# Optimization experiments

Hardware: AMD Instinct MI355X
Metric: run time of the kernel (lower is better)

The kernel has to match this reference:

```python
import jax, jax.numpy as jnp
import numpy as np

B, T, D, H = 2, 2048, 768, 12
HS = D // H


def setup_inputs() -> dict:
    key = jax.random.key(0)
    ks = jax.random.split(key, 11)
    s = 1.0 / np.sqrt(D)
    return {
        "query": jax.random.normal(ks[0], (B, T, D), jnp.float32),
        "key": jax.random.normal(ks[1], (B, T, D), jnp.float32),
        "value": jax.random.normal(ks[2], (B, T, D), jnp.float32),
        "Wq": jax.random.normal(ks[3], (D, D), jnp.float32) * s,
        "bq": jax.random.normal(ks[4], (D,), jnp.float32) * s,
        "Wk": jax.random.normal(ks[5], (D, D), jnp.float32) * s,
        "bk": jax.random.normal(ks[6], (D,), jnp.float32) * s,
        "Wv": jax.random.normal(ks[7], (D, D), jnp.float32) * s,
        "bv": jax.random.normal(ks[8], (D,), jnp.float32) * s,
        "Wo": jax.random.normal(ks[9], (D, D), jnp.float32) * s,
        "bo": jax.random.normal(ks[10], (D,), jnp.float32) * s,
    }


def reference(query, key, value, Wq, bq, Wk, bk, Wv, bv, Wo, bo):
    # Projections (torch nn.Linear: x @ W.T + b), then split heads -> [B,H,T,HS]
    def split_heads(x):
        return x.reshape(B, -1, H, HS).transpose(0, 2, 1, 3)

    q = split_heads(query @ Wq.T + bq)
    k = split_heads(key @ Wk.T + bk)
    v = split_heads(value @ Wv.T + bv)

    scale = 1.0 / jnp.sqrt(jnp.asarray(HS, q.dtype))
    scores = jnp.einsum("bhqd,bhkd->bhqk", q, k) * scale  # [B,H,Tq,Tk]
    attn = jax.nn.softmax(scores, axis=-1)
    out = jnp.einsum("bhqk,bhkd->bhqd", attn, v)  # [B,H,Tq,HS]
    out = out.transpose(0, 2, 1, 3).reshape(B, -1, D)
    output = out @ Wo.T + bo
    return output, attn.mean(axis=1)
```

## Files before the change

### kernel.cpp

```cpp
#include <hip/hip_runtime.h>
#include <hip/hip_fp16.h>
#include <stdint.h>

typedef _Float16 f16;
typedef _Float16 f16x8 __attribute__((ext_vector_type(8)));
typedef _Float16 f16x4v __attribute__((ext_vector_type(4)));
typedef __fp16 h16x2 __attribute__((ext_vector_type(2)));
typedef float f32x4 __attribute__((ext_vector_type(4)));
typedef float f32x16 __attribute__((ext_vector_type(16)));

#define MFMA16(a,b,c) __builtin_amdgcn_mfma_f32_16x16x32_f16(a,b,c,0,0,0)
#define MFMA32(a,b,c) __builtin_amdgcn_mfma_f32_32x32x16_f16(a,b,c,0,0,0)
#define CVTPK(a,b) __builtin_amdgcn_cvt_pkrtz(a,b)

#if __has_builtin(__builtin_amdgcn_exp2f)
#define EXP2(x) __builtin_amdgcn_exp2f(x)
#else
#define EXP2(x) exp2f(x)
#endif

static __device__ __forceinline__ float dot2acc(h16x2 a, float c) {
#if __has_builtin(__builtin_amdgcn_fdot2)
    const h16x2 one = { (__fp16)1.f, (__fp16)1.f };
    return __builtin_amdgcn_fdot2(a, one, c, false);
#else
    return c + (float)a[0] + (float)a[1];
#endif
}

typedef __attribute__((address_space(1))) void gvoid_t;
typedef __attribute__((address_space(3))) void svoid_t;
#define AS1(p) ((gvoid_t*)(uintptr_t)(p))
#define AS3(p) ((svoid_t*)(uint32_t)(uintptr_t)(p))

static constexpr int Bc = 2, Tc = 2048, Dc = 768, Hc = 12;
static constexpr int Mc = Bc * Tc;
static constexpr float SC2 = 0.18033688011112042f;

union PA { f16x8 v; h16x2 h[4]; };

#define FRAG32(BASE, ROWOFF, CHUNK) \
    (*(const f16x8*)((const char*)(BASE) + \
        ((ROWOFF) + q32) * 128 + (((CHUNK) ^ g7) * 16)))

__global__ __launch_bounds__(256) void conv_all(
    const float* __restrict__ q, const float* __restrict__ k, const float* __restrict__ v,
    const float* __restrict__ wq, const float* __restrict__ wk, const float* __restrict__ wv,
    const float* __restrict__ wo,
    f16* __restrict__ qh, f16* __restrict__ kh, f16* __restrict__ vh,
    f16* __restrict__ wqh, f16* __restrict__ wkh, f16* __restrict__ wvh, f16* __restrict__ woh)
{
    const int NI = (Mc * Dc) / 4;
    const int NW = (Dc * Dc) / 4;
    int i = blockIdx.x * 256 + threadIdx.x;
    if (i >= 3 * NI + 4 * NW) return;
    const float4* src; f16* dst; int j; float scl = 1.f;
    if (i < 3 * NI) {
        int a = i / NI; j = i - a * NI;
        src = (const float4*)(a == 0 ? q : (a == 1 ? k : v));
        dst = (a == 0 ? qh : (a == 1 ? kh : vh));
    } else {
        int t = i - 3 * NI;
        int a = t / NW; j = t - a * NW;
        src = (const float4*)(a == 0 ? wq : (a == 1 ? wk : (a == 2 ? wv : wo)));
        dst = (a == 0 ? wqh : (a == 1 ? wkh : (a == 2 ? wvh : woh)));
        if (a == 0) scl = SC2;
    }
    float4 f = src[j];
    f16x4v o = { (f16)(f.x * scl), (f16)(f.y * scl), (f16)(f.z * scl), (f16)(f.w * scl) };
    *(f16x4v*)(dst + 4 * j) = o;
}

__device__ __forceinline__ void gemm_tile_mainloop_db(
    const f16* __restrict__ A, const f16* __restrict__ W,
    int brow, int bcol, f16* As, f16* Bs, f32x4 acc[4][4])
{
    const int tid = threadIdx.x;
    const int w = tid >> 6, lane = tid & 63;
    const int lg = lane & 15, hg = lane >> 4;
    const int wr = w >> 1, wc = w & 1;

#define GS(KT_, BUF_) do { \
    const int k0_ = (KT_) * 32; \
    _Pragma("unroll") \
    for (int j_ = 0; j_ < 2; ++j_) { \
        int p_ = (w * 2 + j_) * 1024 + lane * 16; \
        int r_ = p_ >> 6; \
        int ke_ = (p_ & 63) >> 1; \
        __builtin_amdgcn_global_load_lds(AS1(A + (size_t)(brow + r_) * 768 + k0_ + ke_), \
            AS3((char*)As + (BUF_) * 8192 + (w * 2 + j_) * 1024), 16, 0, 0); \
        __builtin_amdgcn_global_load_lds(AS1(W + (size_t)(bcol + r_) * 768 + k0_ + ke_), \
            AS3((char*)Bs + (BUF_) * 8192 + (w * 2 + j_) * 1024), 16, 0, 0); \
    } } while (0)

    GS(0, 0);
    __syncthreads();
    for (int kt = 0; kt < 24; ++kt) {
        const int cur = kt & 1;
        if (kt < 23) GS(kt + 1, cur ^ 1);
        const f16* As_ = As + cur * 4096;
        const f16* Bs_ = Bs + cur * 4096;
        f16x8 af[4], bf[4];
#pragma unroll
        for (int m = 0; m < 4; ++m)
            af[m] = *(const f16x8*)(As_ + (wr * 64 + m * 16 + lg) * 32 + hg * 8);
#pragma unroll
        for (int n = 0; n < 4; ++n)
            bf[n] = *(const f16x8*)(Bs_ + (wc * 64 + n * 16 + lg) * 32 + hg * 8);
#pragma unroll
        for (int m = 0; m < 4; ++m)
#pragma unroll
            for (int n = 0; n < 4; ++n)
                acc[m][n] = MFMA16(af[m], bf[n], acc[m][n]);
        __syncthreads();
    }
#undef GS
}

__global__ __launch_bounds__(256) void qkv_proj(
    const f16* __restrict__ qh, const f16* __restrict__ kh, const f16* __restrict__ vh,
    const f16* __restrict__ wqh, const f16* __restrict__ wkh, const f16* __restrict__ wvh,
    const float* __restrict__ bq, const float* __restrict__ bk, const float* __restrict__ bv,
    f16* __restrict__ Qp, f16* __restrict__ Kp, f16* __restrict__ Vt)
{
    __shared__ f16 As[2][4096], Bs[2][4096];
    const int z = blockIdx.z;
    const f16* A = (z == 0) ? qh : (z == 1) ? kh : vh;
    const f16* W = (z == 0) ? wqh : (z == 1) ? wkh : wvh;
    const float* bias = (z == 0) ? bq : (z == 1) ? bk : bv;
    const int brow = blockIdx.y * 128, bcol = blockIdx.x * 128;

    f32x4 acc[4][4];
    const f32x4 z4 = { 0.f, 0.f, 0.f, 0.f };
#pragma unroll
    for (int m = 0; m < 4; ++m)
#pragma unroll
        for (int n = 0; n < 4; ++n) acc[m][n] = z4;

    gemm_tile_mainloop_db(A, W, brow, bcol, &As[0][0], &Bs[0][0], acc);

    const int tid = threadIdx.x, w = tid >> 6, lane = tid & 63;
    const int lg = lane & 15, hg = lane >> 4, wr = w >> 1, wc = w & 1;
#pragma unroll
    for (int n = 0; n < 4; ++n) {
        const int c = bcol + wc * 64 + n * 16 + lg;
        const float bval = (z == 0) ? bias[c] * SC2 : bias[c];
#pragma unroll
        for (int m = 0; m < 4; ++m) {
            const int r0 = brow + wr * 64 + m * 16 + hg * 4;
#pragma unroll
            for (int r = 0; r < 4; ++r) {
                const float val = acc[m][n][r] + bval;
                const int row = r0 + r;
                if (z == 0) {
                    Qp[(size_t)row * 768 + c] = (f16)val;
                } else if (z == 1) {
                    Kp[(size_t)row * 768 + c] = (f16)val;
                } else {
                    const int bb = row >> 11, t = row & 2047;
                    const int hh = c >> 6, d = c & 63;
                    const int tl = t & 31;
                    const int sw = ((tl >> 2) ^ (tl >> 3)) & 1;
                    const int tp = (t & ~31) | (tl ^ (sw * 12));
                    Vt[(((size_t)(bb * 12 + hh)) * 64 + d) * 2048 + tp] = (f16)val;
                }
            }
        }
    }
}

__global__ __launch_bounds__(256, 3) void attn_out(
    const f16* __restrict__ Qp, const f16* __restrict__ Kp, const f16* __restrict__ Vt,
    float* __restrict__ l_inv, f16* __restrict__ ctx)
{
    __shared__ f16 Kbuf[2][4096];
    __shared__ f16 Vbuf[2][4096];
    __shared__ float Ored[2][32][64];
    __shared__ float lred[2][2][32];

    const int qt = blockIdx.x, h = blockIdx.y, b = blockIdx.z;
    const int tid = threadIdx.x, w = tid >> 6, lane = tid & 63;
    const int q32 = lane & 31, hi = lane >> 5, g7 = lane & 7;
    const int qh = w & 1, kh = w >> 1;
    const int wbase16 = (tid & ~63) * 16;

    const size_t qrow0 = (size_t)b * 2048 + qt * 64 + qh * 32;
    const int hcol = h * 64;

    const f16* qb = Qp + (qrow0 + q32) * 768 + hcol + hi * 8;
    f16x8 bqf[4];
#pragma unroll
    for (int d = 0; d < 4; ++d) bqf[d] = *(const f16x8*)(qb + d * 16);

    const size_t kbase = (size_t)b * 2048;
    const f16* Vg = Vt + ((size_t)(b * 12 + h)) * 64 * 2048;

    f32x16 oacc[2];
#pragma unroll
    for (int dt = 0; dt < 2; ++dt)
#pragma unroll
        for (int r = 0; r < 16; ++r) oacc[dt][r] = 0.f;
    float lsum = 0.f;

#define STAGE_KV(KT_, BUF) do { \
    _Pragma("unroll") \
    for (int j_ = 0; j_ < 2; ++j_) { \
        const int p_ = j_ * 256 + tid; \
        const int row_ = p_ >> 3, c_ = (p_ & 7) ^ (row_ & 7); \
        __builtin_amdgcn_global_load_lds( \
            AS1(Kp + (kbase + (size_t)(KT_) * 64 + row_) * 768 + hcol + c_ * 8), \
            AS3((char*)&Kbuf[BUF][0] + j_ * 4096 + wbase16), 16, 0, 0); \
        __builtin_amdgcn_global_load_lds( \
            AS1(Vg + (size_t)row_ * 2048 + (KT_) * 64 + c_ * 8), \
            AS3((char*)&Vbuf[BUF][0] + j_ * 4096 + wbase16), 16, 0, 0); \
    } } while (0)

#define AOBODY(CUR) do { \
    const f16* Kb_ = &Kbuf[CUR][0]; const f16* Vb_ = &Vbuf[CUR][0]; \
    f32x16 sa; \
    _Pragma("unroll") \
    for (int r_ = 0; r_ < 16; ++r_) sa[r_] = 0.f; \
    sa = MFMA32(FRAG32(Kb_, kh * 32, 0 + hi), bqf[0], sa); \
    sa = MFMA32(FRAG32(Kb_, kh * 32, 2 + hi), bqf[1], sa); \
    sa = MFMA32(FRAG32(Kb_, kh * 32, 4 + hi), bqf[2], sa); \
    sa = MFMA32(FRAG32(Kb_, kh * 32, 6 + hi), bqf[3], sa); \
    float p[16]; \
    _Pragma("unroll") \
    for (int r_ = 0; r_ < 16; ++r_) p[r_] = EXP2(sa[r_]); \
    PA pa0, pa1; \
    pa0.h[0] = CVTPK(p[0], p[1]);   pa0.h[1] = CVTPK(p[2], p[3]); \
    pa0.h[2] = CVTPK(p[4], p[5]);   pa0.h[3] = CVTPK(p[6], p[7]); \
    pa1.h[0] = CVTPK(p[8], p[9]);   pa1.h[1] = CVTPK(p[10], p[11]); \
    pa1.h[2] = CVTPK(p[12], p[13]); pa1.h[3] = CVTPK(p[14], p[15]); \
    float t0_ = 0.f, t1_ = 0.f; \
    t0_ = dot2acc(pa0.h[0], t0_); t0_ = dot2acc(pa0.h[1], t0_); \
    t0_ = dot2acc(pa0.h[2], t0_); t0_ = dot2acc(pa0.h[3], t0_); \
    t1_ = dot2acc(pa1.h[0], t1_); t1_ = dot2acc(pa1.h[1], t1_); \
    t1_ = dot2acc(pa1.h[2], t1_); t1_ = dot2acc(pa1.h[3], t1_); \
    lsum += t0_ + t1_; \
    oacc[0] = MFMA32(FRAG32(Vb_, 0,  kh * 4 + 0 + hi), pa0.v, oacc[0]); \
    oacc[0] = MFMA32(FRAG32(Vb_, 0,  kh * 4 + 2 + hi), pa1.v, oacc[0]); \
    oacc[1] = MFMA32(FRAG32(Vb_, 32, kh * 4 + 0 + hi), pa0.v, oacc[1]); \
    oacc[1] = MFMA32(FRAG32(Vb_, 32, kh * 4 + 2 + hi), pa1.v, oacc[1]); \
} while (0)

    STAGE_KV(0, 0);
    __syncthreads();
    for (int kt = 0; kt < 32; ++kt) {
        const int cur = kt & 1;
        if (kt < 31) STAGE_KV(kt + 1, cur ^ 1);
        AOBODY(cur);
        __syncthreads();
    }
#undef STAGE_KV
#undef AOBODY

    lsum += __shfl_xor(lsum, 32);
    if (hi == 0) lred[kh][qh][q32] = lsum;
    if (kh == 1) {
#pragma unroll
        for (int dt = 0; dt < 2; ++dt)
#pragma unroll
            for (int g = 0; g < 4; ++g) {
                float4 v4 = { oacc[dt][g * 4 + 0], oacc[dt][g * 4 + 1],
                              oacc[dt][g * 4 + 2], oacc[dt][g * 4 + 3] };
                *(float4*)&Ored[qh][q32][dt * 32 + g * 8 + hi * 4] = v4;
            }
    }
    __syncthreads();
    if (kh == 0) {
        const float iv = 1.f / (lred[0][qh][q32] + lred[1][qh][q32]);
        if (hi == 0)
            l_inv[((size_t)(b * 12 + h)) * 2048 + qt * 64 + qh * 32 + q32] = iv;
        f16* cb = ctx + (qrow0 + q32) * 768 + hcol;
#pragma unroll
        for (int dt = 0; dt < 2; ++dt)
#pragma unroll
            for (int g = 0; g < 4; ++g) {
                const int d0 = dt * 32 + g * 8 + hi * 4;
                const float4 o4 = *(const float4*)&Ored[qh][q32][d0];
                f16x4v s;
#pragma unroll
                for (int e = 0; e < 4; ++e)
                    s[e] = (f16)((oacc[dt][g * 4 + e] + (&o4.x)[e]) * iv);
                *(f16x4v*)(cb + d0) = s;
            }
    }
}

__global__ __launch_bounds__(256) void tail_fused(
    const f16* __restrict__ ctx, const f16* __restrict__ woh,
    const float* __restrict__ bo, float* __restrict__ out,
    const f16* __restrict__ Qp, const f16* __restrict__ Kp,
    const float* __restrict__ l_inv, float* __restrict__ om)
{
    __shared__ f16 sh[4][4096];

    const int tid = threadIdx.x, w = tid >> 6, lane = tid & 63;

    if (blockIdx.x < 192) {
        const int brow = (blockIdx.x / 6) * 128, bcol = (blockIdx.x % 6) * 128;
        f32x4 acc[4][4];
        const f32x4 z4 = { 0.f, 0.f, 0.f, 0.f };
#pragma unroll
        for (int m = 0; m < 4; ++m)
#pragma unroll
            for (int n = 0; n < 4; ++n) acc[m][n] = z4;

        gemm_tile_mainloop_db(ctx, woh, brow, bcol, &sh[0][0], &sh[2][0], acc);

        const int lg = lane & 15, hg = lane >> 4, wr = w >> 1, wc = w & 1;
#pragma unroll
        for (int n = 0; n < 4; ++n) {
            const int c = bcol + wc * 64 + n * 16 + lg;
            const float bval = bo[c];
#pragma unroll
            for (int m = 0; m < 4; ++m) {
                const int r0 = brow + wr * 64 + m * 16 + hg * 4;
#pragma unroll
                for (int r = 0; r < 4; ++r)
                    out[(size_t)(r0 + r) * 768 + c] = acc[m][n][r] + bval;
            }
        }
    } else {
        const int mb = blockIdx.x - 192;
        const int kt = mb & 31, r2 = mb >> 5;
        const int qt = r2 & 31, b = r2 >> 5;
        const int q32 = lane & 31, hi = lane >> 5, g7 = lane & 7;
        const int qh = w & 1, kh = w >> 1;
        const int wbase16 = (tid & ~63) * 16;

        const size_t qtrow = (size_t)b * 2048 + qt * 64;
        const size_t ktrow = (size_t)b * 2048 + kt * 64;

        f32x16 macc;
#pragma unroll
        for (int r = 0; r < 16; ++r) macc[r] = 0.f;

#define MSTAGE(H_, BUF) do { \
    _Pragma("unroll") \
    for (int j_ = 0; j_ < 2; ++j_) { \
        const int p_ = j_ * 256 + tid; \
        const int row_ = p_ >> 3, c_ = (p_ & 7) ^ (row_ & 7); \
        __builtin_amdgcn_global_load_lds( \
            AS1(Qp + (qtrow + row_) * 768 + (H_) * 64 + c_ * 8), \
            AS3((char*)&sh[0][0] + (BUF) * 8192 + j_ * 4096 + wbase16), 16, 0, 0); \
        __builtin_amdgcn_global_load_lds( \
            AS1(Kp + (ktrow + row_) * 768 + (H_) * 64 + c_ * 8), \
            AS3((char*)&sh[2][0] + (BUF) * 8192 + j_ * 4096 + wbase16), 16, 0, 0); \
    } } while (0)

#define MBODY(H_, CUR) do { \
    const f16* Qb_ = (const f16*)((const char*)&sh[0][0] + (CUR) * 8192); \
    const f16* Kb_ = (const f16*)((const char*)&sh[2][0] + (CUR) * 8192); \
    f16x8 qf[4]; \
    _Pragma("unroll") \
    for (int d_ = 0; d_ < 4; ++d_) qf[d_] = FRAG32(Qb_, qh * 32, d_ * 2 + hi); \
    f32x16 sa; \
    _Pragma("unroll") \
    for (int r_ = 0; r_ < 16; ++r_) sa[r_] = 0.f; \
    sa = MFMA32(FRAG32(Kb_, kh * 32, 0 + hi), qf[0], sa); \
    sa = MFMA32(FRAG32(Kb_, kh * 32, 2 + hi), qf[1], sa); \
    sa = MFMA32(FRAG32(Kb_, kh * 32, 4 + hi), qf[2], sa); \
    sa = MFMA32(FRAG32(Kb_, kh * 32, 6 + hi), qf[3], sa); \
    const float ivv = l_inv[((size_t)(b * 12 + (H_))) * 2048 + qt * 64 + qh * 32 + q32]; \
    _Pragma("unroll") \
    for (int r_ = 0; r_ < 16; ++r_) macc[r_] += EXP2(sa[r_]) * ivv; \
} while (0)

        MSTAGE(0, 0);
        __syncthreads();
        for (int h = 0; h < 12; ++h) {
            const int cur = h & 1;
            if (h < 11) MSTAGE(h + 1, cur ^ 1);
            MBODY(h, cur);
            __syncthreads();
        }
#undef MSTAGE
#undef MBODY

        float* ob = om + ((size_t)(b * 2048 + qt * 64 + qh * 32 + q32)) * 2048
                  + kt * 64 + kh * 32;
#pragma unroll
        for (int g = 0; g < 4; ++g) {
            float4 v4 = { macc[g * 4 + 0] * (1.0f / 12.0f),
                          macc[g * 4 + 1] * (1.0f / 12.0f),
                          macc[g * 4 + 2] * (1.0f / 12.0f),
                          macc[g * 4 + 3] * (1.0f / 12.0f) };
            *(float4*)(ob + g * 8 + hi * 4) = v4;
        }
    }
}

extern "C" void kernel_launch(void* const* d_in, const int* in_sizes, int n_in,
                              void* d_out, int out_size, void* d_ws, size_t ws_size,
                              hipStream_t stream) {
    const float* q  = (const float*)d_in[0];
    const float* k  = (const float*)d_in[1];
    const float* v  = (const float*)d_in[2];
    const float* Wq = (const float*)d_in[3];
    const float* bq = (const float*)d_in[4];
    const float* Wk = (const float*)d_in[5];
    const float* bk = (const float*)d_in[6];
    const float* Wv = (const float*)d_in[7];
    const float* bv = (const float*)d_in[8];
    const float* Wo = (const float*)d_in[9];
    const float* bo = (const float*)d_in[10];
    float* out = (float*)d_out;

    char* ws = (char*)d_ws;
    const size_t SZ_IN = (size_t)Mc * Dc * 2;
    const size_t SZ_W  = (size_t)Dc * Dc * 2;
    f16* qh  = (f16*)(ws);
    f16* kh  = (f16*)(ws + SZ_IN);
    f16* vh  = (f16*)(ws + 2 * SZ_IN);
    f16* wqh = (f16*)(ws + 3 * SZ_IN);
    f16* wkh = (f16*)(ws + 3 * SZ_IN + SZ_W);
    f16* wvh = (f16*)(ws + 3 * SZ_IN + 2 * SZ_W);
    f16* woh = (f16*)(ws + 3 * SZ_IN + 3 * SZ_W);
    f16* Qp  = (f16*)(ws + 3 * SZ_IN + 4 * SZ_W);
    f16* Kp  = (f16*)(ws + 4 * SZ_IN + 4 * SZ_W);
    f16* Vt  = (f16*)(ws + 5 * SZ_IN + 4 * SZ_W);
    f16* ctx = qh;
    float* l_inv = (float*)kh;

    conv_all<<<dim3(11520), dim3(256), 0, stream>>>(q, k, v, Wq, Wk, Wv, Wo,
                                                    qh, kh, vh, wqh, wkh, wvh, woh);
    qkv_proj<<<dim3(6, 32, 3), dim3(256), 0, stream>>>(qh, kh, vh, wqh, wkh, wvh,
                                                       bq, bk, bv, Qp, Kp, Vt);
    attn_out<<<dim3(32, 12, 2), dim3(256), 0, stream>>>(Qp, Kp, Vt, l_inv, ctx);
    tail_fused<<<dim3(2240), dim3(256), 0, stream>>>(ctx, woh, bo, out,
                                                     Qp, Kp, l_inv,
                                                     out + (size_t)Mc * Dc);
}
```

Measured before the change: 131.2 us.

## Switch projection GEMMs to 32x32 MFMA with K=64 staging; widen head-mean tiles to 128 keys

The shared projection GEMM mainloop now stages 64-wide K slices with XOR-swizzled LDS layout and uses 32x32x16 MFMA fragments instead of 16x16x32, halving the number of K iterations and barriers. The attention-mean part of the tail kernel now processes 128 key columns per block, reusing each loaded Q head tile for two score tiles and roughly halving the block count. The changes aim to cut LDS traffic per FLOP, barrier count and redundant Q loads, at the cost of doubled LDS per block (which may reduce occupancy) and different epilogue store patterns.

```diff
diff --git a/kernel.cpp b/kernel.cpp
--- a/kernel.cpp
+++ b/kernel.cpp
@@ -9,7 +9,6 @@
 typedef float f32x4 __attribute__((ext_vector_type(4)));
 typedef float f32x16 __attribute__((ext_vector_type(16)));
 
-#define MFMA16(a,b,c) __builtin_amdgcn_mfma_f32_16x16x32_f16(a,b,c,0,0,0)
 #define MFMA32(a,b,c) __builtin_amdgcn_mfma_f32_32x32x16_f16(a,b,c,0,0,0)
 #define CVTPK(a,b) __builtin_amdgcn_cvt_pkrtz(a,b)
 
@@ -42,6 +41,7 @@
 #define FRAG32(BASE, ROWOFF, CHUNK) \
     (*(const f16x8*)((const char*)(BASE) + \
         ((ROWOFF) + q32) * 128 + (((CHUNK) ^ g7) * 16)))
+
 
 __global__ __launch_bounds__(256) void conv_all(
     const float* __restrict__ q, const float* __restrict__ k, const float* __restrict__ v,
@@ -71,50 +71,49 @@
     *(f16x4v*)(dst + 4 * j) = o;
 }
 
-__device__ __forceinline__ void gemm_tile_mainloop_db(
+__device__ __forceinline__ void gemm128_db(
     const f16* __restrict__ A, const f16* __restrict__ W,
-    int brow, int bcol, f16* As, f16* Bs, f32x4 acc[4][4])
+    int brow, int bcol, f16* As, f16* Bs, f32x16 acc[2][2])
 {
     const int tid = threadIdx.x;
     const int w = tid >> 6, lane = tid & 63;
-    const int lg = lane & 15, hg = lane >> 4;
+    const int q32 = lane & 31, hi = lane >> 5, g7 = lane & 7;
     const int wr = w >> 1, wc = w & 1;
-
-#define GS(KT_, BUF_) do { \
-    const int k0_ = (KT_) * 32; \
-    _Pragma("unroll") \
-    for (int j_ = 0; j_ < 2; ++j_) { \
-        int p_ = (w * 2 + j_) * 1024 + lane * 16; \
-        int r_ = p_ >> 6; \
-        int ke_ = (p_ & 63) >> 1; \
-        __builtin_amdgcn_global_load_lds(AS1(A + (size_t)(brow + r_) * 768 + k0_ + ke_), \
-            AS3((char*)As + (BUF_) * 8192 + (w * 2 + j_) * 1024), 16, 0, 0); \
-        __builtin_amdgcn_global_load_lds(AS1(W + (size_t)(bcol + r_) * 768 + k0_ + ke_), \
-            AS3((char*)Bs + (BUF_) * 8192 + (w * 2 + j_) * 1024), 16, 0, 0); \
+    const int wbase16 = (tid & ~63) * 16;
+
+#define GS64(KT_, BUF_) do { \
+    const int k0_ = (KT_) * 64; \
+    _Pragma("unroll") \
+    for (int j_ = 0; j_ < 4; ++j_) { \
+        const int p_ = j_ * 256 + tid; \
+        const int row_ = p_ >> 3, c_ = (p_ & 7) ^ (row_ & 7); \
+        __builtin_amdgcn_global_load_lds(AS1(A + (size_t)(brow + row_) * 768 + k0_ + c_ * 8), \
+            AS3((char*)As + (BUF_) * 16384 + j_ * 4096 + wbase16), 16, 0, 0); \
+        __builtin_amdgcn_global_load_lds(AS1(W + (size_t)(bcol + row_) * 768 + k0_ + c_ * 8), \
+            AS3((char*)Bs + (BUF_) * 16384 + j_ * 4096 + wbase16), 16, 0, 0); \
     } } while (0)
 
-    GS(0, 0);
+    GS64(0, 0);
     __syncthreads();
-    for (int kt = 0; kt < 24; ++kt) {
+    for (int kt = 0; kt < 12; ++kt) {
         const int cur = kt & 1;
-        if (kt < 23) GS(kt + 1, cur ^ 1);
-        const f16* As_ = As + cur * 4096;
-        const f16* Bs_ = Bs + cur * 4096;
-        f16x8 af[4], bf[4];
-#pragma unroll
-        for (int m = 0; m < 4; ++m)
-            af[m] = *(const f16x8*)(As_ + (wr * 64 + m * 16 + lg) * 32 + hg * 8);
-#pragma unroll
-        for (int n = 0; n < 4; ++n)
-            bf[n] = *(const f16x8*)(Bs_ + (wc * 64 + n * 16 + lg) * 32 + hg * 8);
-#pragma unroll
-        for (int m = 0; m < 4; ++m)
-#pragma unroll
-            for (int n = 0; n < 4; ++n)
-                acc[m][n] = MFMA16(af[m], bf[n], acc[m][n]);
+        if (kt < 11) GS64(kt + 1, cur ^ 1);
+        const f16* As_ = As + cur * 8192;
+        const f16* Bs_ = Bs + cur * 8192;
+#pragma unroll
+        for (int ks = 0; ks < 4; ++ks) {
+            const f16x8 af0 = FRAG32(As_, wr * 64,      ks * 2 + hi);
+            const f16x8 af1 = FRAG32(As_, wr * 64 + 32, ks * 2 + hi);
+            const f16x8 bf0 = FRAG32(Bs_, wc * 64,      ks * 2 + hi);
+            const f16x8 bf1 = FRAG32(Bs_, wc * 64 + 32, ks * 2 + hi);
+            acc[0][0] = MFMA32(af0, bf0, acc[0][0]);
+            acc[0][1] = MFMA32(af0, bf1, acc[0][1]);
+            acc[1][0] = MFMA32(af1, bf0, acc[1][0]);
+            acc[1][1] = MFMA32(af1, bf1, acc[1][1]);
+        }
         __syncthreads();
     }
-#undef GS
+#undef GS64
 }
 
 __global__ __launch_bounds__(256) void qkv_proj(
@@ -123,35 +122,36 @@
     const float* __restrict__ bq, const float* __restrict__ bk, const float* __restrict__ bv,
     f16* __restrict__ Qp, f16* __restrict__ Kp, f16* __restrict__ Vt)
 {
-    __shared__ f16 As[2][4096], Bs[2][4096];
+    __shared__ f16 As[2][8192], Bs[2][8192];
     const int z = blockIdx.z;
     const f16* A = (z == 0) ? qh : (z == 1) ? kh : vh;
     const f16* W = (z == 0) ? wqh : (z == 1) ? wkh : wvh;
     const float* bias = (z == 0) ? bq : (z == 1) ? bk : bv;
     const int brow = blockIdx.y * 128, bcol = blockIdx.x * 128;
 
-    f32x4 acc[4][4];
-    const f32x4 z4 = { 0.f, 0.f, 0.f, 0.f };
-#pragma unroll
-    for (int m = 0; m < 4; ++m)
-#pragma unroll
-        for (int n = 0; n < 4; ++n) acc[m][n] = z4;
-
-    gemm_tile_mainloop_db(A, W, brow, bcol, &As[0][0], &Bs[0][0], acc);
+    f32x16 acc[2][2];
+#pragma unroll
+    for (int mi = 0; mi < 2; ++mi)
+#pragma unroll
+        for (int ni = 0; ni < 2; ++ni)
+#pragma unroll
+            for (int r = 0; r < 16; ++r) acc[mi][ni][r] = 0.f;
+
+    gemm128_db(A, W, brow, bcol, &As[0][0], &Bs[0][0], acc);
 
     const int tid = threadIdx.x, w = tid >> 6, lane = tid & 63;
-    const int lg = lane & 15, hg = lane >> 4, wr = w >> 1, wc = w & 1;
-#pragma unroll
-    for (int n = 0; n < 4; ++n) {
-        const int c = bcol + wc * 64 + n * 16 + lg;
+    const int q32 = lane & 31, hi = lane >> 5;
+    const int wr = w >> 1, wc = w & 1;
+#pragma unroll
+    for (int ni = 0; ni < 2; ++ni) {
+        const int c = bcol + wc * 64 + ni * 32 + q32;
         const float bval = (z == 0) ? bias[c] * SC2 : bias[c];
 #pragma unroll
-        for (int m = 0; m < 4; ++m) {
-            const int r0 = brow + wr * 64 + m * 16 + hg * 4;
-#pragma unroll
-            for (int r = 0; r < 4; ++r) {
-                const float val = acc[m][n][r] + bval;
-                const int row = r0 + r;
+        for (int mi = 0; mi < 2; ++mi) {
+#pragma unroll
+            for (int r = 0; r < 16; ++r) {
+                const int row = brow + wr * 64 + mi * 32 + (r & 3) + 8 * (r >> 2) + 4 * hi;
+                const float val = acc[mi][ni][r] + bval;
                 if (z == 0) {
                     Qp[(size_t)row * 768 + c] = (f16)val;
                 } else if (z == 1) {
@@ -294,48 +294,53 @@
     const f16* __restrict__ Qp, const f16* __restrict__ Kp,
     const float* __restrict__ l_inv, float* __restrict__ om)
 {
-    __shared__ f16 sh[4][4096];
+    __shared__ f16 sh[32768];
 
     const int tid = threadIdx.x, w = tid >> 6, lane = tid & 63;
+    const int q32 = lane & 31, hi = lane >> 5, g7 = lane & 7;
+    const int wbase16 = (tid & ~63) * 16;
 
     if (blockIdx.x < 192) {
         const int brow = (blockIdx.x / 6) * 128, bcol = (blockIdx.x % 6) * 128;
-        f32x4 acc[4][4];
-        const f32x4 z4 = { 0.f, 0.f, 0.f, 0.f };
-#pragma unroll
-        for (int m = 0; m < 4; ++m)
-#pragma unroll
-            for (int n = 0; n < 4; ++n) acc[m][n] = z4;
-
-        gemm_tile_mainloop_db(ctx, woh, brow, bcol, &sh[0][0], &sh[2][0], acc);
-
-        const int lg = lane & 15, hg = lane >> 4, wr = w >> 1, wc = w & 1;
-#pragma unroll
-        for (int n = 0; n < 4; ++n) {
-            const int c = bcol + wc * 64 + n * 16 + lg;
+        f32x16 acc[2][2];
+#pragma unroll
+        for (int mi = 0; mi < 2; ++mi)
+#pragma unroll
+            for (int ni = 0; ni < 2; ++ni)
+#pragma unroll
+                for (int r = 0; r < 16; ++r) acc[mi][ni][r] = 0.f;
+
+        gemm128_db(ctx, woh, brow, bcol, sh, sh + 16384, acc);
+
+        const int wr = w >> 1, wc = w & 1;
+#pragma unroll
+        for (int ni = 0; ni < 2; ++ni) {
+            const int c = bcol + wc * 64 + ni * 32 + q32;
             const float bval = bo[c];
 #pragma unroll
-            for (int m = 0; m < 4; ++m) {
-                const int r0 = brow + wr * 64 + m * 16 + hg * 4;
-#pragma unroll
-                for (int r = 0; r < 4; ++r)
-                    out[(size_t)(r0 + r) * 768 + c] = acc[m][n][r] + bval;
+            for (int mi = 0; mi < 2; ++mi) {
+#pragma unroll
+                for (int r = 0; r < 16; ++r) {
+                    const int row = brow + wr * 64 + mi * 32 + (r & 3) + 8 * (r >> 2) + 4 * hi;
+                    out[(size_t)row * 768 + c] = acc[mi][ni][r] + bval;
+                }
             }
         }
     } else {
         const int mb = blockIdx.x - 192;
-        const int kt = mb & 31, r2 = mb >> 5;
+        const int kt2 = mb & 15, r2 = mb >> 4;
         const int qt = r2 & 31, b = r2 >> 5;
-        const int q32 = lane & 31, hi = lane >> 5, g7 = lane & 7;
         const int qh = w & 1, kh = w >> 1;
-        const int wbase16 = (tid & ~63) * 16;
+
+        f16* Qb = sh;
+        f16* Kb = sh + 8192;
 
         const size_t qtrow = (size_t)b * 2048 + qt * 64;
-        const size_t ktrow = (size_t)b * 2048 + kt * 64;
-
-        f32x16 macc;
-#pragma unroll
-        for (int r = 0; r < 16; ++r) macc[r] = 0.f;
+        const size_t ktrow = (size_t)b * 2048 + kt2 * 128;
+
+        f32x16 macc0, macc1;
+#pragma unroll
+        for (int r = 0; r < 16; ++r) { macc0[r] = 0.f; macc1[r] = 0.f; }
 
 #define MSTAGE(H_, BUF) do { \
     _Pragma("unroll") \
@@ -344,28 +349,36 @@
         const int row_ = p_ >> 3, c_ = (p_ & 7) ^ (row_ & 7); \
         __builtin_amdgcn_global_load_lds( \
             AS1(Qp + (qtrow + row_) * 768 + (H_) * 64 + c_ * 8), \
-            AS3((char*)&sh[0][0] + (BUF) * 8192 + j_ * 4096 + wbase16), 16, 0, 0); \
+            AS3((char*)Qb + (BUF) * 8192 + j_ * 4096 + wbase16), 16, 0, 0); \
+    } \
+    _Pragma("unroll") \
+    for (int j_ = 0; j_ < 4; ++j_) { \
+        const int p_ = j_ * 256 + tid; \
+        const int row_ = p_ >> 3, c_ = (p_ & 7) ^ (row_ & 7); \
         __builtin_amdgcn_global_load_lds( \
             AS1(Kp + (ktrow + row_) * 768 + (H_) * 64 + c_ * 8), \
-            AS3((char*)&sh[2][0] + (BUF) * 8192 + j_ * 4096 + wbase16), 16, 0, 0); \
+            AS3((char*)Kb + (BUF) * 16384 + j_ * 4096 + wbase16), 16, 0, 0); \
     } } while (0)
 
 #define MBODY(H_, CUR) do { \
-    const f16* Qb_ = (const f16*)((const char*)&sh[0][0] + (CUR) * 8192); \
-    const f16* Kb_ = (const f16*)((const char*)&sh[2][0] + (CUR) * 8192); \
+    const f16* Qb_ = (const f16*)((const char*)Qb + (CUR) * 8192); \
+    const f16* Kb_ = (const f16*)((const char*)Kb + (CUR) * 16384); \
     f16x8 qf[4]; \
     _Pragma("unroll") \
     for (int d_ = 0; d_ < 4; ++d_) qf[d_] = FRAG32(Qb_, qh * 32, d_ * 2 + hi); \
-    f32x16 sa; \
-    _Pragma("unroll") \
-    for (int r_ = 0; r_ < 16; ++r_) sa[r_] = 0.f; \
-    sa = MFMA32(FRAG32(Kb_, kh * 32, 0 + hi), qf[0], sa); \
-    sa = MFMA32(FRAG32(Kb_, kh * 32, 2 + hi), qf[1], sa); \
-    sa = MFMA32(FRAG32(Kb_, kh * 32, 4 + hi), qf[2], sa); \
-    sa = MFMA32(FRAG32(Kb_, kh * 32, 6 + hi), qf[3], sa); \
+    f32x16 sa0, sa1; \
+    _Pragma("unroll") \
+    for (int r_ = 0; r_ < 16; ++r_) { sa0[r_] = 0.f; sa1[r_] = 0.f; } \
+    _Pragma("unroll") \
+    for (int d_ = 0; d_ < 4; ++d_) { \
+        sa0 = MFMA32(FRAG32(Kb_, kh * 64,      d_ * 2 + hi), qf[d_], sa0); \
+        sa1 = MFMA32(FRAG32(Kb_, kh * 64 + 32, d_ * 2 + hi), qf[d_], sa1); \
+    } \
     const float ivv = l_inv[((size_t)(b * 12 + (H_))) * 2048 + qt * 64 + qh * 32 + q32]; \
     _Pragma("unroll") \
-    for (int r_ = 0; r_ < 16; ++r_) macc[r_] += EXP2(sa[r_]) * ivv; \
+    for (int r_ = 0; r_ < 16; ++r_) { \
+        macc0[r_] += EXP2(sa0[r_]) * ivv; \
+        macc1[r_] += EXP2(sa1[r_]) * ivv; } \
 } while (0)
 
         MSTAGE(0, 0);
@@ -380,14 +393,19 @@
 #undef MBODY
 
         float* ob = om + ((size_t)(b * 2048 + qt * 64 + qh * 32 + q32)) * 2048
-                  + kt * 64 + kh * 32;
+                  + kt2 * 128 + kh * 64;
 #pragma unroll
         for (int g = 0; g < 4; ++g) {
-            float4 v4 = { macc[g * 4 + 0] * (1.0f / 12.0f),
-                          macc[g * 4 + 1] * (1.0f / 12.0f),
-                          macc[g * 4 + 2] * (1.0f / 12.0f),
-                          macc[g * 4 + 3] * (1.0f / 12.0f) };
-            *(float4*)(ob + g * 8 + hi * 4) = v4;
+            float4 v0 = { macc0[g * 4 + 0] * (1.0f / 12.0f),
+                          macc0[g * 4 + 1] * (1.0f / 12.0f),
+                          macc0[g * 4 + 2] * (1.0f / 12.0f),
+                          macc0[g * 4 + 3] * (1.0f / 12.0f) };
+            *(float4*)(ob + g * 8 + hi * 4) = v0;
+            float4 v1 = { macc1[g * 4 + 0] * (1.0f / 12.0f),
+                          macc1[g * 4 + 1] * (1.0f / 12.0f),
+                          macc1[g * 4 + 2] * (1.0f / 12.0f),
+                          macc1[g * 4 + 3] * (1.0f / 12.0f) };
+            *(float4*)(ob + 32 + g * 8 + hi * 4) = v1;
         }
     }
 }
@@ -429,7 +447,7 @@
     qkv_proj<<<dim3(6, 32, 3), dim3(256), 0, stream>>>(qh, kh, vh, wqh, wkh, wvh,
                                                        bq, bk, bv, Qp, Kp, Vt);
     attn_out<<<dim3(32, 12, 2), dim3(256), 0, stream>>>(Qp, Kp, Vt, l_inv, ctx);
-    tail_fused<<<dim3(2240), dim3(256), 0, stream>>>(ctx, woh, bo, out,
+    tail_fused<<<dim3(1216), dim3(256), 0, stream>>>(ctx, woh, bo, out,
                                                      Qp, Kp, l_inv,
                                                      out + (size_t)Mc * Dc);
 }
```

Measured after the change: 134.4 us. 2.4% more time.

## Switch projection GEMMs to 128x64 tiles with 32x32 MFMA and swizzled LDS

Applied to the files above, without the earlier changes.

The shared GEMM mainloop now uses 128x64 output tiles with 32x32x16 MFMA instructions in place of 128x128 tiles with 16x16x32 MFMA. Operands are staged into LDS in an XOR-swizzled paired-row layout to avoid bank conflicts. The V projection epilogue now transposes through LDS and writes Vt with vectorised 16-byte stores instead of scattered 2-byte stores. Grids double for qkv_proj and the out-projection part of tail_fused, raising block count and occupancy at the cost of lower per-block operand reuse.

```diff
diff --git a/kernel.cpp b/kernel.cpp
--- a/kernel.cpp
+++ b/kernel.cpp
@@ -9,7 +9,6 @@
 typedef float f32x4 __attribute__((ext_vector_type(4)));
 typedef float f32x16 __attribute__((ext_vector_type(16)));
 
-#define MFMA16(a,b,c) __builtin_amdgcn_mfma_f32_16x16x32_f16(a,b,c,0,0,0)
 #define MFMA32(a,b,c) __builtin_amdgcn_mfma_f32_32x32x16_f16(a,b,c,0,0,0)
 #define CVTPK(a,b) __builtin_amdgcn_cvt_pkrtz(a,b)
 
@@ -42,6 +41,11 @@
 #define FRAG32(BASE, ROWOFF, CHUNK) \
     (*(const f16x8*)((const char*)(BASE) + \
         ((ROWOFF) + q32) * 128 + (((CHUNK) ^ g7) * 16)))
+
+#define FRAGP(BASE, ROWOFF, C) \
+    (*(const f16x8*)((const char*)(BASE) + \
+        (((ROWOFF) / 2 + (q32 >> 1)) * 128) + \
+        (((((q32 & 1) << 2) | (C)) ^ ((q32 >> 1) & 7)) * 16)))
 
 __global__ __launch_bounds__(256) void conv_all(
     const float* __restrict__ q, const float* __restrict__ k, const float* __restrict__ v,
@@ -71,50 +75,53 @@
     *(f16x4v*)(dst + 4 * j) = o;
 }
 
-__device__ __forceinline__ void gemm_tile_mainloop_db(
+__device__ __forceinline__ void gemm_bk32(
     const f16* __restrict__ A, const f16* __restrict__ W,
-    int brow, int bcol, f16* As, f16* Bs, f32x4 acc[4][4])
+    int brow, int bcol, char* As, char* Bs, f32x16 acc[2])
 {
     const int tid = threadIdx.x;
     const int w = tid >> 6, lane = tid & 63;
-    const int lg = lane & 15, hg = lane >> 4;
+    const int q32 = lane & 31, hi = lane >> 5;
     const int wr = w >> 1, wc = w & 1;
-
-#define GS(KT_, BUF_) do { \
+    const int wbase16 = (tid & ~63) * 16;
+
+#define GSA(KT_, BUF_) do { \
     const int k0_ = (KT_) * 32; \
     _Pragma("unroll") \
     for (int j_ = 0; j_ < 2; ++j_) { \
-        int p_ = (w * 2 + j_) * 1024 + lane * 16; \
-        int r_ = p_ >> 6; \
-        int ke_ = (p_ & 63) >> 1; \
-        __builtin_amdgcn_global_load_lds(AS1(A + (size_t)(brow + r_) * 768 + k0_ + ke_), \
-            AS3((char*)As + (BUF_) * 8192 + (w * 2 + j_) * 1024), 16, 0, 0); \
-        __builtin_amdgcn_global_load_lds(AS1(W + (size_t)(bcol + r_) * 768 + k0_ + ke_), \
-            AS3((char*)Bs + (BUF_) * 8192 + (w * 2 + j_) * 1024), 16, 0, 0); \
+        const int p_ = j_ * 256 + tid; \
+        const int L_ = p_ >> 3, c8_ = (p_ & 7) ^ (L_ & 7); \
+        const int row_ = 2 * L_ + (c8_ >> 2), kc_ = (c8_ & 3) * 8; \
+        __builtin_amdgcn_global_load_lds(AS1(A + (size_t)(brow + row_) * 768 + k0_ + kc_), \
+            AS3(As + (BUF_) * 8192 + j_ * 4096 + wbase16), 16, 0, 0); \
     } } while (0)
-
-    GS(0, 0);
+#define GSB(KT_, BUF_) do { \
+    const int k0_ = (KT_) * 32; \
+    const int L_ = tid >> 3, c8_ = (tid & 7) ^ (L_ & 7); \
+    const int row_ = 2 * L_ + (c8_ >> 2), kc_ = (c8_ & 3) * 8; \
+    __builtin_amdgcn_global_load_lds(AS1(W + (size_t)(bcol + row_) * 768 + k0_ + kc_), \
+        AS3(Bs + (BUF_) * 4096 + wbase16), 16, 0, 0); \
+    } while (0)
+
+    GSA(0, 0); GSB(0, 0);
     __syncthreads();
     for (int kt = 0; kt < 24; ++kt) {
         const int cur = kt & 1;
-        if (kt < 23) GS(kt + 1, cur ^ 1);
-        const f16* As_ = As + cur * 4096;
-        const f16* Bs_ = Bs + cur * 4096;
-        f16x8 af[4], bf[4];
-#pragma unroll
-        for (int m = 0; m < 4; ++m)
-            af[m] = *(const f16x8*)(As_ + (wr * 64 + m * 16 + lg) * 32 + hg * 8);
-#pragma unroll
-        for (int n = 0; n < 4; ++n)
-            bf[n] = *(const f16x8*)(Bs_ + (wc * 64 + n * 16 + lg) * 32 + hg * 8);
-#pragma unroll
-        for (int m = 0; m < 4; ++m)
-#pragma unroll
-            for (int n = 0; n < 4; ++n)
-                acc[m][n] = MFMA16(af[m], bf[n], acc[m][n]);
+        if (kt < 23) { GSA(kt + 1, cur ^ 1); GSB(kt + 1, cur ^ 1); }
+        const char* As_ = As + cur * 8192;
+        const char* Bs_ = Bs + cur * 4096;
+#pragma unroll
+        for (int ks = 0; ks < 2; ++ks) {
+            const f16x8 af0 = FRAGP(As_, wr * 64,      ks * 2 + hi);
+            const f16x8 af1 = FRAGP(As_, wr * 64 + 32, ks * 2 + hi);
+            const f16x8 bf  = FRAGP(Bs_, wc * 32,      ks * 2 + hi);
+            acc[0] = MFMA32(af0, bf, acc[0]);
+            acc[1] = MFMA32(af1, bf, acc[1]);
+        }
         __syncthreads();
     }
-#undef GS
+#undef GSA
+#undef GSB
 }
 
 __global__ __launch_bounds__(256) void qkv_proj(
@@ -123,48 +130,61 @@
     const float* __restrict__ bq, const float* __restrict__ bk, const float* __restrict__ bv,
     f16* __restrict__ Qp, f16* __restrict__ Kp, f16* __restrict__ Vt)
 {
-    __shared__ f16 As[2][4096], Bs[2][4096];
+    __shared__ char lds[24576];
+    char* As = lds; char* Bs = lds + 16384;
+
     const int z = blockIdx.z;
     const f16* A = (z == 0) ? qh : (z == 1) ? kh : vh;
     const f16* W = (z == 0) ? wqh : (z == 1) ? wkh : wvh;
     const float* bias = (z == 0) ? bq : (z == 1) ? bk : bv;
-    const int brow = blockIdx.y * 128, bcol = blockIdx.x * 128;
-
-    f32x4 acc[4][4];
-    const f32x4 z4 = { 0.f, 0.f, 0.f, 0.f };
-#pragma unroll
-    for (int m = 0; m < 4; ++m)
-#pragma unroll
-        for (int n = 0; n < 4; ++n) acc[m][n] = z4;
-
-    gemm_tile_mainloop_db(A, W, brow, bcol, &As[0][0], &Bs[0][0], acc);
+    const int brow = blockIdx.y * 128, bcol = blockIdx.x * 64;
+
+    f32x16 acc[2];
+#pragma unroll
+    for (int mi = 0; mi < 2; ++mi)
+#pragma unroll
+        for (int r = 0; r < 16; ++r) acc[mi][r] = 0.f;
+
+    gemm_bk32(A, W, brow, bcol, As, Bs, acc);
 
     const int tid = threadIdx.x, w = tid >> 6, lane = tid & 63;
-    const int lg = lane & 15, hg = lane >> 4, wr = w >> 1, wc = w & 1;
-#pragma unroll
-    for (int n = 0; n < 4; ++n) {
-        const int c = bcol + wc * 64 + n * 16 + lg;
-        const float bval = (z == 0) ? bias[c] * SC2 : bias[c];
-#pragma unroll
-        for (int m = 0; m < 4; ++m) {
-            const int r0 = brow + wr * 64 + m * 16 + hg * 4;
-#pragma unroll
-            for (int r = 0; r < 4; ++r) {
-                const float val = acc[m][n][r] + bval;
-                const int row = r0 + r;
-                if (z == 0) {
-                    Qp[(size_t)row * 768 + c] = (f16)val;
-                } else if (z == 1) {
-                    Kp[(size_t)row * 768 + c] = (f16)val;
-                } else {
-                    const int bb = row >> 11, t = row & 2047;
-                    const int hh = c >> 6, d = c & 63;
-                    const int tl = t & 31;
-                    const int sw = ((tl >> 2) ^ (tl >> 3)) & 1;
-                    const int tp = (t & ~31) | (tl ^ (sw * 12));
-                    Vt[(((size_t)(bb * 12 + hh)) * 64 + d) * 2048 + tp] = (f16)val;
-                }
+    const int q32 = lane & 31, hi = lane >> 5;
+    const int wr = w >> 1, wc = w & 1;
+    const int c = bcol + wc * 32 + q32;
+    const float bval = (z == 0) ? bias[c] * SC2 : bias[c];
+
+    if (z < 2) {
+        f16* dst = (z == 0) ? Qp : Kp;
+#pragma unroll
+        for (int mi = 0; mi < 2; ++mi)
+#pragma unroll
+            for (int r = 0; r < 16; ++r) {
+                const int row = brow + wr * 64 + mi * 32 + (r & 3) + 8 * (r >> 2) + 4 * hi;
+                dst[(size_t)row * 768 + c] = (f16)(acc[mi][r] + bval);
             }
+    } else {
+        __syncthreads();
+        const int dl = wc * 32 + q32;
+#pragma unroll
+        for (int mi = 0; mi < 2; ++mi)
+#pragma unroll
+            for (int j = 0; j < 8; ++j) {
+                const int r0 = 2 * j;
+                const int crow = (r0 & 3) + 8 * (r0 >> 2) + 4 * hi;
+                const int sw = ((crow >> 2) ^ (crow >> 3)) & 1;
+                const int tp = crow ^ (sw * 12);
+                const int tloc = wr * 64 + mi * 32 + tp;
+                const h16x2 pv = CVTPK(acc[mi][r0] + bval, acc[mi][r0 + 1] + bval);
+                *(h16x2*)(As + dl * 256 + ((tloc * 2) ^ ((dl & 7) << 4))) = pv;
+            }
+        __syncthreads();
+        const int bb = brow >> 11, t0 = brow & 2047, hh = bcol >> 6;
+        f16* Vh = Vt + ((size_t)(bb * 12 + hh) * 64) * 2048;
+#pragma unroll
+        for (int j = 0; j < 4; ++j) {
+            const int dr = j * 16 + (tid >> 4), off = tid & 15;
+            const f16x8 vv = *(const f16x8*)(As + dr * 256 + ((off * 16) ^ ((dr & 7) << 4)));
+            *(f16x8*)(Vh + (size_t)dr * 2048 + t0 + off * 8) = vv;
         }
     }
 }
@@ -294,41 +314,40 @@
     const f16* __restrict__ Qp, const f16* __restrict__ Kp,
     const float* __restrict__ l_inv, float* __restrict__ om)
 {
-    __shared__ f16 sh[4][4096];
+    __shared__ char sh[32768];
 
     const int tid = threadIdx.x, w = tid >> 6, lane = tid & 63;
-
-    if (blockIdx.x < 192) {
-        const int brow = (blockIdx.x / 6) * 128, bcol = (blockIdx.x % 6) * 128;
-        f32x4 acc[4][4];
-        const f32x4 z4 = { 0.f, 0.f, 0.f, 0.f };
-#pragma unroll
-        for (int m = 0; m < 4; ++m)
-#pragma unroll
-            for (int n = 0; n < 4; ++n) acc[m][n] = z4;
-
-        gemm_tile_mainloop_db(ctx, woh, brow, bcol, &sh[0][0], &sh[2][0], acc);
-
-        const int lg = lane & 15, hg = lane >> 4, wr = w >> 1, wc = w & 1;
-#pragma unroll
-        for (int n = 0; n < 4; ++n) {
-            const int c = bcol + wc * 64 + n * 16 + lg;
-            const float bval = bo[c];
-#pragma unroll
-            for (int m = 0; m < 4; ++m) {
-                const int r0 = brow + wr * 64 + m * 16 + hg * 4;
-#pragma unroll
-                for (int r = 0; r < 4; ++r)
-                    out[(size_t)(r0 + r) * 768 + c] = acc[m][n][r] + bval;
+    const int q32 = lane & 31, hi = lane >> 5, g7 = lane & 7;
+    const int wbase16 = (tid & ~63) * 16;
+
+    if (blockIdx.x < 384) {
+        const int brow = (blockIdx.x / 12) * 128, bcol = (blockIdx.x % 12) * 64;
+        f32x16 acc[2];
+#pragma unroll
+        for (int mi = 0; mi < 2; ++mi)
+#pragma unroll
+            for (int r = 0; r < 16; ++r) acc[mi][r] = 0.f;
+
+        gemm_bk32(ctx, woh, brow, bcol, sh, sh + 16384, acc);
+
+        const int wr = w >> 1, wc = w & 1;
+        const int c = bcol + wc * 32 + q32;
+        const float bval = bo[c];
+#pragma unroll
+        for (int mi = 0; mi < 2; ++mi)
+#pragma unroll
+            for (int r = 0; r < 16; ++r) {
+                const int row = brow + wr * 64 + mi * 32 + (r & 3) + 8 * (r >> 2) + 4 * hi;
+                out[(size_t)row * 768 + c] = acc[mi][r] + bval;
             }
-        }
     } else {
-        const int mb = blockIdx.x - 192;
+        const int mb = blockIdx.x - 384;
         const int kt = mb & 31, r2 = mb >> 5;
         const int qt = r2 & 31, b = r2 >> 5;
-        const int q32 = lane & 31, hi = lane >> 5, g7 = lane & 7;
         const int qh = w & 1, kh = w >> 1;
-        const int wbase16 = (tid & ~63) * 16;
+
+        char* Qb = sh;
+        char* Kb = sh + 16384;
 
         const size_t qtrow = (size_t)b * 2048 + qt * 64;
         const size_t ktrow = (size_t)b * 2048 + kt * 64;
@@ -344,15 +363,15 @@
         const int row_ = p_ >> 3, c_ = (p_ & 7) ^ (row_ & 7); \
         __builtin_amdgcn_global_load_lds( \
             AS1(Qp + (qtrow + row_) * 768 + (H_) * 64 + c_ * 8), \
-            AS3((char*)&sh[0][0] + (BUF) * 8192 + j_ * 4096 + wbase16), 16, 0, 0); \
+            AS3(Qb + (BUF) * 8192 + j_ * 4096 + wbase16), 16, 0, 0); \
         __builtin_amdgcn_global_load_lds( \
             AS1(Kp + (ktrow + row_) * 768 + (H_) * 64 + c_ * 8), \
-            AS3((char*)&sh[2][0] + (BUF) * 8192 + j_ * 4096 + wbase16), 16, 0, 0); \
+            AS3(Kb + (BUF) * 8192 + j_ * 4096 + wbase16), 16, 0, 0); \
     } } while (0)
 
 #define MBODY(H_, CUR) do { \
-    const f16* Qb_ = (const f16*)((const char*)&sh[0][0] + (CUR) * 8192); \
-    const f16* Kb_ = (const f16*)((const char*)&sh[2][0] + (CUR) * 8192); \
+    const f16* Qb_ = (const f16*)(Qb + (CUR) * 8192); \
+    const f16* Kb_ = (const f16*)(Kb + (CUR) * 8192); \
     f16x8 qf[4]; \
     _Pragma("unroll") \
     for (int d_ = 0; d_ < 4; ++d_) qf[d_] = FRAG32(Qb_, qh * 32, d_ * 2 + hi); \
@@ -426,10 +445,10 @@
 
     conv_all<<<dim3(11520), dim3(256), 0, stream>>>(q, k, v, Wq, Wk, Wv, Wo,
                                                     qh, kh, vh, wqh, wkh, wvh, woh);
-    qkv_proj<<<dim3(6, 32, 3), dim3(256), 0, stream>>>(qh, kh, vh, wqh, wkh, wvh,
-                                                       bq, bk, bv, Qp, Kp, Vt);
+    qkv_proj<<<dim3(12, 32, 3), dim3(256), 0, stream>>>(qh, kh, vh, wqh, wkh, wvh,
+                                                        bq, bk, bv, Qp, Kp, Vt);
     attn_out<<<dim3(32, 12, 2), dim3(256), 0, stream>>>(Qp, Kp, Vt, l_inv, ctx);
-    tail_fused<<<dim3(2240), dim3(256), 0, stream>>>(ctx, woh, bo, out,
+    tail_fused<<<dim3(2432), dim3(256), 0, stream>>>(ctx, woh, bo, out,
                                                      Qp, Kp, l_inv,
                                                      out + (size_t)Mc * Dc);
 }
```

Result: no change. 130.0 us (-0.9%).
